# Performance work log

Hardware: AMD Instinct MI355X
Metric: run time of the kernel (lower is better)

The kernel has to match this reference:

```python
import jax, jax.numpy as jnp
import numpy as np

# ---- config matching init_kwargs ----
B, D, U = 8192, 1024, 512
F, E, T = 4, 4, 2
MAX_VAL = 10000000000.0
MIN_VAL = -10000000000.0
DISC_IDX = np.array([[0, 1, 2, 3], [4, 5, 6, 7]])  # discrete fields 0,1: per-expert feature index
CONT_IDX = np.array([8, 9])                         # continuous fields 2,3: single feature index
BOUNDS = np.array([-0.5, 0.0, 0.5])                 # 3 boundaries -> 4 buckets per continuous field
LOWERS = np.concatenate([[MIN_VAL], BOUNDS]).astype(np.float32)
UPPERS = np.concatenate([BOUNDS, [MAX_VAL]]).astype(np.float32)


def setup_inputs() -> dict:
    key = jax.random.key(0)
    ks = jax.random.split(key, 8)
    s_in = 1.0 / np.sqrt(D)
    s_cat = 1.0 / np.sqrt(2 * U)
    x = jax.random.normal(ks[0], (B, D), dtype=jnp.float32)
    Wc = jax.random.normal(ks[1], (D, U), dtype=jnp.float32) * s_in      # common expert kernel
    bc = jnp.zeros((U,), dtype=jnp.float32)
    We = jax.random.normal(ks[2], (F, E, D, U), dtype=jnp.float32) * s_in  # per-field per-expert kernels
    be = jnp.zeros((F, E, U), dtype=jnp.float32)
    Wg = jax.random.normal(ks[3], (T, D, F + 1), dtype=jnp.float32) * s_in  # per-task gate kernels
    bg = jnp.zeros((T, F + 1), dtype=jnp.float32)
    Wa = jax.random.normal(ks[4], (F, 2 * U, 1), dtype=jnp.float32) * s_cat  # attention kernels
    ba = jnp.zeros((F, 1), dtype=jnp.float32)
    Wu = jax.random.normal(ks[5], (F, 2 * U, 1), dtype=jnp.float32) * s_cat  # update kernels
    bu = jnp.zeros((F, 1), dtype=jnp.float32)
    return {"x": x, "Wc": Wc, "bc": bc, "We": We, "be": be,
            "Wg": Wg, "bg": bg, "Wa": Wa, "ba": ba, "Wu": Wu, "bu": bu}


def _field_masks(x):
    # discrete fields: expert j active iff x[:, idx[i][j]] > 0
    m_disc = x[:, DISC_IDX] > 0.0                         # [B, 2, E]
    # continuous fields: bucket x[:, idx] by boundaries (lower < v <= upper)
    v = x[:, CONT_IDX][..., None]                         # [B, 2, 1]
    m_cont = (v > LOWERS) & (v <= UPPERS)                 # [B, 2, E]
    return jnp.concatenate([m_disc, m_cont], axis=1).astype(x.dtype)  # [B, F, E]


def reference(x, Wc, bc, We, be, Wg, bg, Wa, ba, Wu, bu):
    # common expert: [B, U]
    common = jax.nn.relu(x @ Wc + bc)
    # all field experts at once: [B, F, E, U]
    e = jax.nn.relu(jnp.einsum('bd,fedu->bfeu', x, We) + be)
    mask = _field_masks(x)                                # [B, F, E]
    # mask-select active expert(s) per field: [B, F, U]
    field_out = jnp.einsum('bfe,bfeu->bfu', mask, e)
    # concat [common, field] per field: [B, F, 2U]
    cat = jnp.concatenate(
        [jnp.broadcast_to(common[:, None, :], field_out.shape), field_out], axis=-1)
    # sigmoid attention reweights field expert output
    att = jax.nn.sigmoid(jnp.einsum('bfk,fko->bfo', cat, Wa) + ba[None])   # [B, F, 1]
    field_att = att * field_out
    # sigmoid update gate blends field expert with common expert
    upd = jax.nn.sigmoid(jnp.einsum('bfk,fko->bfo', cat, Wu) + bu[None])   # [B, F, 1]
    field_final = upd * field_att + (1.0 - upd) * common[:, None, :]       # [B, F, U]
    # experts = [common] + per-field outputs: [B, F+1, U]
    experts = jnp.concatenate([common[:, None, :], field_final], axis=1)
    # per-task softmax gates over F+1 experts: [B, T, F+1]
    gates = jax.nn.softmax(jnp.einsum('bd,tdg->btg', x, Wg) + bg[None], axis=-1)
    # task outputs: [B, T, U]
    return jnp.einsum('btg,bgu->btu', gates, experts)
```

## Files before the change

### kernel.cpp

```cpp
#include <hip/hip_runtime.h>

typedef unsigned short ushort_t;

#define B_SZ 8192
#define D_SZ 1024
#define U_SZ 512
#define F_SZ 4
#define E_SZ 4
#define T_SZ 2

typedef __attribute__((ext_vector_type(8))) short bf16x8;
typedef __attribute__((ext_vector_type(4))) float f32x4;
typedef __attribute__((ext_vector_type(8))) unsigned short u16x8;

__device__ __forceinline__ unsigned short f2bf(float f) {
  union { float f; unsigned int u; } v; v.f = f;
  unsigned int r = v.u + 0x7FFFu + ((v.u >> 16) & 1u);
  return (unsigned short)(r >> 16);
}
__device__ __forceinline__ float bf2f(unsigned short h) {
  union { unsigned int u; float f; } v; v.u = ((unsigned int)h) << 16;
  return v.f;
}

__device__ __forceinline__ void gload_lds16(const void* g, void* l) {
  __builtin_amdgcn_global_load_lds(
      (const __attribute__((address_space(1))) unsigned int*)g,
      (__attribute__((address_space(3))) unsigned int*)l, 16, 0, 0);
}

__global__ __launch_bounds__(256) void conv_x(const float* __restrict__ x,
                                              ushort_t* __restrict__ xbf,
                                              float* __restrict__ mask) {
  const size_t i = ((size_t)blockIdx.x * 256 + threadIdx.x) * 8;
  const float4 a = *(const float4*)(x + i);
  const float4 c = *(const float4*)(x + i + 4);
  u16x8 o;
  o[0] = f2bf(a.x); o[1] = f2bf(a.y); o[2] = f2bf(a.z); o[3] = f2bf(a.w);
  o[4] = f2bf(c.x); o[5] = f2bf(c.y); o[6] = f2bf(c.z); o[7] = f2bf(c.w);
  *(u16x8*)(xbf + i) = o;

  if ((threadIdx.x & 127) == 0) {
    const int b = blockIdx.x * 2 + (threadIdx.x >> 7);
    const float* xr = x + (size_t)b * D_SZ;
    float m[16];
    m[0] = a.x > 0.f ? 1.f : 0.f; m[1] = a.y > 0.f ? 1.f : 0.f;
    m[2] = a.z > 0.f ? 1.f : 0.f; m[3] = a.w > 0.f ? 1.f : 0.f;
    m[4] = c.x > 0.f ? 1.f : 0.f; m[5] = c.y > 0.f ? 1.f : 0.f;
    m[6] = c.z > 0.f ? 1.f : 0.f; m[7] = c.w > 0.f ? 1.f : 0.f;
    const float LO[4] = {-1e10f, -0.5f, 0.f, 0.5f};
    const float HI[4] = {-0.5f, 0.f, 0.5f, 1e10f};
    const float v0 = xr[8], v1 = xr[9];
#pragma unroll
    for (int j = 0; j < 4; ++j) {
      m[8 + j]  = ((v0 > LO[j]) && (v0 <= HI[j])) ? 1.f : 0.f;
      m[12 + j] = ((v1 > LO[j]) && (v1 <= HI[j])) ? 1.f : 0.f;
    }
#pragma unroll
    for (int k = 0; k < 4; ++k) {
      float4 v4 = {m[k * 4], m[k * 4 + 1], m[k * 4 + 2], m[k * 4 + 3]};
      *(float4*)(mask + (size_t)b * 16 + k * 4) = v4;
    }
  }
}

__global__ __launch_bounds__(256) void conv_w(const float* __restrict__ Wc,
                                              const float* __restrict__ We,
                                              ushort_t* __restrict__ wbf) {
  const int blk = blockIdx.x;
  const int midx = blk >> 7;
  const int tid = blk & 127;
  const int trow = (tid >> 3) * 64;
  const int tcol = (tid & 7) * 64;
  const float* src = (midx == 0) ? Wc : (We + (size_t)(midx - 1) * D_SZ * U_SZ);
  ushort_t* dst = wbf + (size_t)midx * U_SZ * D_SZ;

  __shared__ float tile[64][69];
  const int t = threadIdx.x;
  const int r0 = t >> 2;
  const int cseg = (t & 3) * 16;
#pragma unroll
  for (int j = 0; j < 4; ++j) {
    const float4 v = *(const float4*)(src + (size_t)(trow + r0) * U_SZ + tcol + cseg + j * 4);
    tile[r0][cseg + j * 4 + 0] = v.x;
    tile[r0][cseg + j * 4 + 1] = v.y;
    tile[r0][cseg + j * 4 + 2] = v.z;
    tile[r0][cseg + j * 4 + 3] = v.w;
  }
  __syncthreads();
  const int u = t >> 2;
  const int d0 = (t & 3) * 16;
#pragma unroll
  for (int h = 0; h < 2; ++h) {
    u16x8 ov;
#pragma unroll
    for (int k = 0; k < 8; ++k) ov[k] = f2bf(tile[d0 + h * 8 + k][u]);
    *(u16x8*)(dst + (size_t)(tcol + u) * D_SZ + trow + d0 + h * 8) = ov;
  }
}

__global__ __launch_bounds__(256) void gates_k(const float* __restrict__ x,
                                               const float* __restrict__ Wg,
                                               const float* __restrict__ bg,
                                               float* __restrict__ gates) {
  __shared__ float wgT[10 * 1024];
  const int t = threadIdx.x;
#pragma unroll
  for (int j = 0; j < 40; ++j) {
    const int i = j * 256 + t;
    const int t2 = i / 5120;
    const int rem = i - t2 * 5120;
    const int d = rem / 5;
    const int g = rem - d * 5;
    wgT[(t2 * 5 + g) * 1024 + d] = Wg[i];
  }
  __syncthreads();
  const int lane = t & 63;
  const int w = t >> 6;
#pragma unroll
  for (int rr = 0; rr < 2; ++rr) {
    const int b = blockIdx.x * 8 + w * 2 + rr;
    const float* xr = x + (size_t)b * D_SZ;
    float p[10];
#pragma unroll
    for (int j = 0; j < 10; ++j) p[j] = 0.f;
#pragma unroll
    for (int i = 0; i < 4; ++i) {
      const int d0 = i * 256 + lane * 4;
      const float4 xv = *(const float4*)(xr + d0);
#pragma unroll
      for (int g = 0; g < 10; ++g) {
        const float4 wv = *(const float4*)(wgT + g * 1024 + d0);
        p[g] += xv.x * wv.x + xv.y * wv.y + xv.z * wv.z + xv.w * wv.w;
      }
    }
#pragma unroll
    for (int off = 32; off > 0; off >>= 1)
#pragma unroll
      for (int j = 0; j < 10; ++j) p[j] += __shfl_xor(p[j], off);
    float l[10];
#pragma unroll
    for (int j = 0; j < 10; ++j) l[j] = p[j] + bg[j];
    const float mx0 = fmaxf(fmaxf(fmaxf(l[0], l[1]), fmaxf(l[2], l[3])), l[4]);
    const float mx1 = fmaxf(fmaxf(fmaxf(l[5], l[6]), fmaxf(l[7], l[8])), l[9]);
    float ev[10]; float s0 = 0.f, s1 = 0.f;
#pragma unroll
    for (int g = 0; g < 5; ++g) { ev[g] = expf(l[g] - mx0); s0 += ev[g]; }
#pragma unroll
    for (int g = 5; g < 10; ++g) { ev[g] = expf(l[g] - mx1); s1 += ev[g]; }
    if (lane < 5) gates[(size_t)b * 10 + lane] = ev[lane] / s0;
    else if (lane < 10) gates[(size_t)b * 10 + lane] = ev[lane] / s1;
  }
}

__global__ __launch_bounds__(256, 2) void gemm_fused(
    const ushort_t* __restrict__ xbf, const ushort_t* __restrict__ wbf,
    const float* __restrict__ mask, const float* __restrict__ bc,
    const float* __restrict__ be,
    ushort_t* __restrict__ common, ushort_t* __restrict__ fout) {
  __shared__ ushort_t Ash[128 * 64];
  __shared__ ushort_t Bsh[128 * 64];
  __shared__ float mk[128 * 4];

  const int t = threadIdx.x;
  const int lane = t & 63;
  const int w = t >> 6;
  const int wm = w >> 1;
  const int wn = w & 1;
  const int quad = lane >> 4;
  const int l16 = lane & 15;
  const int m0 = blockIdx.x * 128;
  const int grp = blockIdx.y;
  const bool isCommon = grp >= 16;
  const int f = isCommon ? 0 : (grp >> 2);
  const int uc = isCommon ? (grp - 16) : (grp & 3);
  const int u0 = uc * 128;
  const int nExp = isCommon ? 1 : 4;
  const int midx0 = isCommon ? 0 : (1 + f * 4);

  if (!isCommon && t < 128)
    *(float4*)(&mk[t * 4]) = *(const float4*)(mask + (size_t)(m0 + t) * 16 + f * 4);

  int offs[4];
#pragma unroll
  for (int i = 0; i < 4; ++i) {
    const int c = (w * 4 + i) * 64 + lane;
    const int r = c >> 3;
    const int gc = (c & 7) ^ (r & 7);
    offs[i] = r * D_SZ + gc * 8;
  }
  const ushort_t* xbase = xbf + (size_t)m0 * D_SZ;

  int rowA[4], rowB[4];
#pragma unroll
  for (int i = 0; i < 4; ++i) {
    rowA[i] = wm * 64 + i * 16 + l16;
    rowB[i] = wn * 64 + i * 16 + l16;
  }
  int sw[2];
  sw[0] = ((quad) ^ (l16 & 7)) * 8;
  sw[1] = ((4 + quad) ^ (l16 & 7)) * 8;

  const f32x4 fzero = {0.f, 0.f, 0.f, 0.f};
  f32x4 facc[4][4];
#pragma unroll
  for (int mi = 0; mi < 4; ++mi)
#pragma unroll
    for (int ni = 0; ni < 4; ++ni) facc[mi][ni] = fzero;

  for (int e = 0; e < nExp; ++e) {
    const ushort_t* wbase = wbf + (size_t)(midx0 + e) * (U_SZ * D_SZ) + (size_t)u0 * D_SZ;
    f32x4 acc[4][4];
#pragma unroll
    for (int mi = 0; mi < 4; ++mi)
#pragma unroll
      for (int ni = 0; ni < 4; ++ni) acc[mi][ni] = fzero;

    for (int k0 = 0; k0 < D_SZ; k0 += 64) {
#pragma unroll
      for (int i = 0; i < 4; ++i) {
        gload_lds16(xbase + offs[i] + k0, (char*)Ash + (w * 4 + i) * 1024);
        gload_lds16(wbase + offs[i] + k0, (char*)Bsh + (w * 4 + i) * 1024);
      }
      __syncthreads();
#pragma unroll
      for (int qs = 0; qs < 2; ++qs) {
        bf16x8 av[4], bv[4];
#pragma unroll
        for (int mi = 0; mi < 4; ++mi)
          av[mi] = *(const bf16x8*)(Ash + rowA[mi] * 64 + sw[qs]);
#pragma unroll
        for (int ni = 0; ni < 4; ++ni)
          bv[ni] = *(const bf16x8*)(Bsh + rowB[ni] * 64 + sw[qs]);
#pragma unroll
        for (int mi = 0; mi < 4; ++mi)
#pragma unroll
          for (int ni = 0; ni < 4; ++ni)
            acc[mi][ni] = __builtin_amdgcn_mfma_f32_16x16x32_bf16(av[mi], bv[ni],
                                                                  acc[mi][ni], 0, 0, 0);
      }
      __syncthreads();
    }

    if (isCommon) {
#pragma unroll
      for (int mi = 0; mi < 4; ++mi) {
        const int rowb = m0 + wm * 64 + mi * 16 + quad * 4;
#pragma unroll
        for (int ni = 0; ni < 4; ++ni) {
          const int u = u0 + wn * 64 + ni * 16 + l16;
          const float bcv = bc[u];
#pragma unroll
          for (int r = 0; r < 4; ++r) {
            const float v = fmaxf(acc[mi][ni][r] + bcv, 0.f);
            common[(size_t)(rowb + r) * U_SZ + u] = f2bf(v);
          }
        }
      }
    } else {
#pragma unroll
      for (int ni = 0; ni < 4; ++ni) {
        const int u = u0 + wn * 64 + ni * 16 + l16;
        const float bev = be[(f * 4 + e) * U_SZ + u];
#pragma unroll
        for (int mi = 0; mi < 4; ++mi) {
          const int rowl = wm * 64 + mi * 16 + quad * 4;
#pragma unroll
          for (int r = 0; r < 4; ++r) {
            const float mval = mk[(rowl + r) * 4 + e];
            const float v = fmaxf(acc[mi][ni][r] + bev, 0.f);
            facc[mi][ni][r] += mval * v;
          }
        }
      }
    }
  }

  if (!isCommon) {
#pragma unroll
    for (int mi = 0; mi < 4; ++mi) {
      const int rowl = wm * 64 + mi * 16 + quad * 4;
#pragma unroll
      for (int ni = 0; ni < 4; ++ni) {
        const int u = u0 + wn * 64 + ni * 16 + l16;
#pragma unroll
        for (int r = 0; r < 4; ++r)
          fout[((size_t)(m0 + rowl + r) * F_SZ + f) * U_SZ + u] = f2bf(facc[mi][ni][r]);
      }
    }
  }
}

__global__ __launch_bounds__(256) void stage2_k(
    const ushort_t* __restrict__ common, const ushort_t* __restrict__ fout,
    const float* __restrict__ gates,
    const float* __restrict__ Wa, const float* __restrict__ ba,
    const float* __restrict__ Wu, const float* __restrict__ bu,
    float* __restrict__ out) {
  const int b = blockIdx.x;
  const int t = threadIdx.x;
  const int lane = t & 63;
  const int w = t >> 6;

  const float c0 = bf2f(common[(size_t)b * U_SZ + t]);
  const float c1 = bf2f(common[(size_t)b * U_SZ + 256 + t]);
  float fo0[4], fo1[4];
#pragma unroll
  for (int f = 0; f < 4; ++f) {
    fo0[f] = bf2f(fout[((size_t)b * F_SZ + f) * U_SZ + t]);
    fo1[f] = bf2f(fout[((size_t)b * F_SZ + f) * U_SZ + 256 + t]);
  }
  float pa[4], pu[4];
#pragma unroll
  for (int f = 0; f < 4; ++f) {
    const float* wa = Wa + f * 1024;
    pa[f] = c0 * wa[t] + c1 * wa[256 + t] + fo0[f] * wa[512 + t] + fo1[f] * wa[768 + t];
    const float* wu = Wu + f * 1024;
    pu[f] = c0 * wu[t] + c1 * wu[256 + t] + fo0[f] * wu[512 + t] + fo1[f] * wu[768 + t];
  }
#pragma unroll
  for (int off = 32; off > 0; off >>= 1) {
#pragma unroll
    for (int f = 0; f < 4; ++f) {
      pa[f] += __shfl_xor(pa[f], off);
      pu[f] += __shfl_xor(pu[f], off);
    }
  }
  __shared__ float redA[4][4];
  __shared__ float redU[4][4];
  __shared__ float gsh[10];
  if (lane == 0) {
#pragma unroll
    for (int f = 0; f < 4; ++f) { redA[w][f] = pa[f]; redU[w][f] = pu[f]; }
  }
  if (t < 10) gsh[t] = gates[(size_t)b * 10 + t];
  __syncthreads();
  float att[4], upd[4], ff0[4], ff1[4];
#pragma unroll
  for (int f = 0; f < 4; ++f) {
    const float sa = redA[0][f] + redA[1][f] + redA[2][f] + redA[3][f] + ba[f];
    const float su = redU[0][f] + redU[1][f] + redU[2][f] + redU[3][f] + bu[f];
    att[f] = 1.f / (1.f + expf(-sa));
    upd[f] = 1.f / (1.f + expf(-su));
    ff0[f] = upd[f] * (att[f] * fo0[f]) + (1.f - upd[f]) * c0;
    ff1[f] = upd[f] * (att[f] * fo1[f]) + (1.f - upd[f]) * c1;
  }
#pragma unroll
  for (int t2 = 0; t2 < 2; ++t2) {
    float v0 = gsh[t2 * 5] * c0;
    float v1 = gsh[t2 * 5] * c1;
#pragma unroll
    for (int f = 0; f < 4; ++f) {
      v0 += gsh[t2 * 5 + 1 + f] * ff0[f];
      v1 += gsh[t2 * 5 + 1 + f] * ff1[f];
    }
    out[((size_t)b * T_SZ + t2) * U_SZ + t] = v0;
    out[((size_t)b * T_SZ + t2) * U_SZ + 256 + t] = v1;
  }
}

extern "C" void kernel_launch(void* const* d_in, const int* in_sizes, int n_in,
                              void* d_out, int out_size, void* d_ws, size_t ws_size,
                              hipStream_t stream) {
  (void)in_sizes; (void)n_in; (void)out_size; (void)ws_size;
  const float* x  = (const float*)d_in[0];
  const float* Wc = (const float*)d_in[1];
  const float* bc = (const float*)d_in[2];
  const float* We = (const float*)d_in[3];
  const float* be = (const float*)d_in[4];
  const float* Wg = (const float*)d_in[5];
  const float* bg = (const float*)d_in[6];
  const float* Wa = (const float*)d_in[7];
  const float* ba = (const float*)d_in[8];
  const float* Wu = (const float*)d_in[9];
  const float* bu = (const float*)d_in[10];
  float* out = (float*)d_out;
  char* ws = (char*)d_ws;

  const size_t O_XBF    = 0;
  const size_t O_WBF    = O_XBF + (size_t)B_SZ * D_SZ * 2;
  const size_t O_MASK   = O_WBF + (size_t)17 * U_SZ * D_SZ * 2;
  const size_t O_GATES  = O_MASK + (size_t)B_SZ * 16 * 4;
  const size_t O_COMMON = O_GATES + (size_t)B_SZ * 10 * 4;
  const size_t O_FOUT   = O_COMMON + (size_t)B_SZ * U_SZ * 2;

  ushort_t* xbf    = (ushort_t*)(ws + O_XBF);
  ushort_t* wbf    = (ushort_t*)(ws + O_WBF);
  float*    maskp  = (float*)(ws + O_MASK);
  float*    gatesp = (float*)(ws + O_GATES);
  ushort_t* commonp= (ushort_t*)(ws + O_COMMON);
  ushort_t* foutp  = (ushort_t*)(ws + O_FOUT);

  conv_x<<<dim3(4096), dim3(256), 0, stream>>>(x, xbf, maskp);
  conv_w<<<dim3(17 * 128), dim3(256), 0, stream>>>(Wc, We, wbf);
  gates_k<<<dim3(1024), dim3(256), 0, stream>>>(x, Wg, bg, gatesp);
  gemm_fused<<<dim3(64, 20), dim3(256), 0, stream>>>(xbf, wbf, maskp, bc, be, commonp, foutp);
  stage2_k<<<dim3(8192), dim3(256), 0, stream>>>(commonp, foutp, gatesp, Wa, ba, Wu, bu, out);
}
```

Measured before the change: 328.4 us.

## Group rows by active-expert pattern and compute only active experts per field

```diff
diff --git a/kernel.cpp b/kernel.cpp
--- a/kernel.cpp
+++ b/kernel.cpp
@@ -29,9 +29,15 @@
       (__attribute__((address_space(3))) unsigned int*)l, 16, 0, 0);
 }
 
+__global__ __launch_bounds__(64) void zero_k(int* __restrict__ cnt) {
+  cnt[threadIdx.x] = 0;
+}
+
 __global__ __launch_bounds__(256) void conv_x(const float* __restrict__ x,
                                               ushort_t* __restrict__ xbf,
-                                              float* __restrict__ mask) {
+                                              unsigned int* __restrict__ pat,
+                                              int* __restrict__ rowidx,
+                                              int* __restrict__ cnt) {
   const size_t i = ((size_t)blockIdx.x * 256 + threadIdx.x) * 8;
   const float4 a = *(const float4*)(x + i);
   const float4 c = *(const float4*)(x + i + 4);
@@ -43,24 +49,46 @@
   if ((threadIdx.x & 127) == 0) {
     const int b = blockIdx.x * 2 + (threadIdx.x >> 7);
     const float* xr = x + (size_t)b * D_SZ;
-    float m[16];
-    m[0] = a.x > 0.f ? 1.f : 0.f; m[1] = a.y > 0.f ? 1.f : 0.f;
-    m[2] = a.z > 0.f ? 1.f : 0.f; m[3] = a.w > 0.f ? 1.f : 0.f;
-    m[4] = c.x > 0.f ? 1.f : 0.f; m[5] = c.y > 0.f ? 1.f : 0.f;
-    m[6] = c.z > 0.f ? 1.f : 0.f; m[7] = c.w > 0.f ? 1.f : 0.f;
+    int p0 = 0, p1 = 0, p2 = 0, p3 = 0;
+    p0 |= (a.x > 0.f) << 0; p0 |= (a.y > 0.f) << 1;
+    p0 |= (a.z > 0.f) << 2; p0 |= (a.w > 0.f) << 3;
+    p1 |= (c.x > 0.f) << 0; p1 |= (c.y > 0.f) << 1;
+    p1 |= (c.z > 0.f) << 2; p1 |= (c.w > 0.f) << 3;
     const float LO[4] = {-1e10f, -0.5f, 0.f, 0.5f};
     const float HI[4] = {-0.5f, 0.f, 0.5f, 1e10f};
     const float v0 = xr[8], v1 = xr[9];
 #pragma unroll
     for (int j = 0; j < 4; ++j) {
-      m[8 + j]  = ((v0 > LO[j]) && (v0 <= HI[j])) ? 1.f : 0.f;
-      m[12 + j] = ((v1 > LO[j]) && (v1 <= HI[j])) ? 1.f : 0.f;
-    }
-#pragma unroll
-    for (int k = 0; k < 4; ++k) {
-      float4 v4 = {m[k * 4], m[k * 4 + 1], m[k * 4 + 2], m[k * 4 + 3]};
-      *(float4*)(mask + (size_t)b * 16 + k * 4) = v4;
-    }
+      if ((v0 > LO[j]) && (v0 <= HI[j])) p2 = 1 << j;
+      if ((v1 > LO[j]) && (v1 <= HI[j])) p3 = 1 << j;
+    }
+    pat[b] = (unsigned int)(p0 | (p1 << 4) | (p2 << 8) | (p3 << 12));
+    int pp[4] = {p0, p1, p2, p3};
+#pragma unroll
+    for (int f = 0; f < 4; ++f) {
+      if (pp[f]) {
+        const int pos = atomicAdd(&cnt[f * 16 + pp[f]], 1);
+        rowidx[((size_t)f * 16 + pp[f]) * B_SZ + pos] = b;
+      }
+    }
+  }
+}
+
+__global__ __launch_bounds__(64) void dir_k(const int* __restrict__ cnt,
+                                            int* __restrict__ dir,
+                                            int* __restrict__ ntiles) {
+  const int f = threadIdx.x;
+  if (f < 4) {
+    int idx = 0;
+    for (int pop = 4; pop >= 1; --pop) {
+      for (int p = 1; p < 16; ++p) {
+        if (__popc(p) != pop) continue;
+        const int n = cnt[f * 16 + p];
+        const int nt = (n + 127) >> 7;
+        for (int k = 0; k < nt; ++k) dir[f * 80 + idx++] = p | (k << 8);
+      }
+    }
+    ntiles[f] = idx;
   }
 }
 
@@ -153,14 +181,15 @@
   }
 }
 
-__global__ __launch_bounds__(256, 2) void gemm_fused(
+__global__ __launch_bounds__(256, 2) void gemm2(
     const ushort_t* __restrict__ xbf, const ushort_t* __restrict__ wbf,
-    const float* __restrict__ mask, const float* __restrict__ bc,
-    const float* __restrict__ be,
+    const int* __restrict__ rowidx, const int* __restrict__ cnt,
+    const int* __restrict__ dir, const int* __restrict__ ntiles,
+    const float* __restrict__ bc, const float* __restrict__ be,
     ushort_t* __restrict__ common, ushort_t* __restrict__ fout) {
   __shared__ ushort_t Ash[128 * 64];
   __shared__ ushort_t Bsh[128 * 64];
-  __shared__ float mk[128 * 4];
+  __shared__ int ridx[128];
 
   const int t = threadIdx.x;
   const int lane = t & 63;
@@ -169,27 +198,40 @@
   const int wn = w & 1;
   const int quad = lane >> 4;
   const int l16 = lane & 15;
-  const int m0 = blockIdx.x * 128;
-  const int grp = blockIdx.y;
-  const bool isCommon = grp >= 16;
-  const int f = isCommon ? 0 : (grp >> 2);
-  const int uc = isCommon ? (grp - 16) : (grp & 3);
-  const int u0 = uc * 128;
-  const int nExp = isCommon ? 1 : 4;
-  const int midx0 = isCommon ? 0 : (1 + f * 4);
-
-  if (!isCommon && t < 128)
-    *(float4*)(&mk[t * 4]) = *(const float4*)(mask + (size_t)(m0 + t) * 16 + f * 4);
-
-  int offs[4];
+  const int f = blockIdx.y;
+  const int slot = blockIdx.x;
+  const int u0 = blockIdx.z * 128;
+  const bool isCommon = (f == 4);
+
+  int p = 0, nrows = 128;
+  if (isCommon) {
+    if (slot >= 64) return;
+    if (t < 128) ridx[t] = slot * 128 + t;
+  } else {
+    if (slot >= ntiles[f]) return;
+    const int entry = dir[f * 80 + slot];
+    p = entry & 15;
+    const int tw = entry >> 8;
+    const int n = cnt[f * 16 + p];
+    const int rbase = tw * 128;
+    nrows = min(128, n - rbase);
+    if (t < 128) {
+      const int rr = rbase + ((t < nrows) ? t : 0);
+      ridx[t] = rowidx[((size_t)f * 16 + p) * B_SZ + rr];
+    }
+  }
+  __syncthreads();
+
+  size_t aoff[4]; int boff[4]; int ldsoff[4];
 #pragma unroll
   for (int i = 0; i < 4; ++i) {
     const int c = (w * 4 + i) * 64 + lane;
     const int r = c >> 3;
     const int gc = (c & 7) ^ (r & 7);
-    offs[i] = r * D_SZ + gc * 8;
-  }
-  const ushort_t* xbase = xbf + (size_t)m0 * D_SZ;
+    aoff[i] = (size_t)ridx[r] * D_SZ + gc * 8;
+    boff[i] = r * D_SZ + gc * 8;
+    ldsoff[i] = (w * 4 + i) * 1024;
+  }
 
   int rowA[4], rowB[4];
 #pragma unroll
@@ -201,6 +243,14 @@
   sw[0] = ((quad) ^ (l16 & 7)) * 8;
   sw[1] = ((4 + quad) ^ (l16 & 7)) * 8;
 
+  int elist[4]; int ne = 0;
+  if (isCommon) { elist[0] = 0; ne = 1; }
+  else {
+#pragma unroll
+    for (int e = 0; e < 4; ++e)
+      if (p & (1 << e)) elist[ne++] = e;
+  }
+
   const f32x4 fzero = {0.f, 0.f, 0.f, 0.f};
   f32x4 facc[4][4];
 #pragma unroll
@@ -208,8 +258,9 @@
 #pragma unroll
     for (int ni = 0; ni < 4; ++ni) facc[mi][ni] = fzero;
 
-  for (int e = 0; e < nExp; ++e) {
-    const ushort_t* wbase = wbf + (size_t)(midx0 + e) * (U_SZ * D_SZ) + (size_t)u0 * D_SZ;
+  for (int ei = 0; ei < ne; ++ei) {
+    const int midx = isCommon ? 0 : (1 + f * 4 + elist[ei]);
+    const ushort_t* wbase = wbf + (size_t)midx * (U_SZ * D_SZ) + (size_t)u0 * D_SZ;
     f32x4 acc[4][4];
 #pragma unroll
     for (int mi = 0; mi < 4; ++mi)
@@ -219,8 +270,8 @@
     for (int k0 = 0; k0 < D_SZ; k0 += 64) {
 #pragma unroll
       for (int i = 0; i < 4; ++i) {
-        gload_lds16(xbase + offs[i] + k0, (char*)Ash + (w * 4 + i) * 1024);
-        gload_lds16(wbase + offs[i] + k0, (char*)Bsh + (w * 4 + i) * 1024);
+        gload_lds16(xbf + aoff[i] + k0, (char*)Ash + ldsoff[i]);
+        gload_lds16(wbase + boff[i] + k0, (char*)Bsh + ldsoff[i]);
       }
       __syncthreads();
 #pragma unroll
@@ -245,7 +296,7 @@
     if (isCommon) {
 #pragma unroll
       for (int mi = 0; mi < 4; ++mi) {
-        const int rowb = m0 + wm * 64 + mi * 16 + quad * 4;
+        const int rowb = slot * 128 + wm * 64 + mi * 16 + quad * 4;
 #pragma unroll
         for (int ni = 0; ni < 4; ++ni) {
           const int u = u0 + wn * 64 + ni * 16 + l16;
@@ -258,42 +309,42 @@
         }
       }
     } else {
+      const float* bevp = be + (size_t)(f * 4 + elist[ei]) * U_SZ;
 #pragma unroll
       for (int ni = 0; ni < 4; ++ni) {
         const int u = u0 + wn * 64 + ni * 16 + l16;
-        const float bev = be[(f * 4 + e) * U_SZ + u];
-#pragma unroll
-        for (int mi = 0; mi < 4; ++mi) {
-          const int rowl = wm * 64 + mi * 16 + quad * 4;
-#pragma unroll
-          for (int r = 0; r < 4; ++r) {
-            const float mval = mk[(rowl + r) * 4 + e];
-            const float v = fmaxf(acc[mi][ni][r] + bev, 0.f);
-            facc[mi][ni][r] += mval * v;
+        const float bev = bevp[u];
+#pragma unroll
+        for (int mi = 0; mi < 4; ++mi)
+#pragma unroll
+          for (int r = 0; r < 4; ++r)
+            facc[mi][ni][r] += fmaxf(acc[mi][ni][r] + bev, 0.f);
+      }
+    }
+  }
+
+  if (!isCommon) {
+#pragma unroll
+    for (int mi = 0; mi < 4; ++mi) {
+      const int rowl = wm * 64 + mi * 16 + quad * 4;
+#pragma unroll
+      for (int r = 0; r < 4; ++r) {
+        if (rowl + r < nrows) {
+          const int brow = ridx[rowl + r];
+#pragma unroll
+          for (int ni = 0; ni < 4; ++ni) {
+            const int u = u0 + wn * 64 + ni * 16 + l16;
+            fout[((size_t)brow * F_SZ + f) * U_SZ + u] = f2bf(facc[mi][ni][r]);
           }
         }
       }
     }
   }
-
-  if (!isCommon) {
-#pragma unroll
-    for (int mi = 0; mi < 4; ++mi) {
-      const int rowl = wm * 64 + mi * 16 + quad * 4;
-#pragma unroll
-      for (int ni = 0; ni < 4; ++ni) {
-        const int u = u0 + wn * 64 + ni * 16 + l16;
-#pragma unroll
-        for (int r = 0; r < 4; ++r)
-          fout[((size_t)(m0 + rowl + r) * F_SZ + f) * U_SZ + u] = f2bf(facc[mi][ni][r]);
-      }
-    }
-  }
 }
 
 __global__ __launch_bounds__(256) void stage2_k(
     const ushort_t* __restrict__ common, const ushort_t* __restrict__ fout,
-    const float* __restrict__ gates,
+    const unsigned int* __restrict__ pat, const float* __restrict__ gates,
     const float* __restrict__ Wa, const float* __restrict__ ba,
     const float* __restrict__ Wu, const float* __restrict__ bu,
     float* __restrict__ out) {
@@ -301,14 +352,16 @@
   const int t = threadIdx.x;
   const int lane = t & 63;
   const int w = t >> 6;
+  const unsigned int pv = pat[b];
 
   const float c0 = bf2f(common[(size_t)b * U_SZ + t]);
   const float c1 = bf2f(common[(size_t)b * U_SZ + 256 + t]);
   float fo0[4], fo1[4];
 #pragma unroll
   for (int f = 0; f < 4; ++f) {
-    fo0[f] = bf2f(fout[((size_t)b * F_SZ + f) * U_SZ + t]);
-    fo1[f] = bf2f(fout[((size_t)b * F_SZ + f) * U_SZ + 256 + t]);
+    const bool act = ((pv >> (4 * f)) & 15u) != 0u;
+    fo0[f] = act ? bf2f(fout[((size_t)b * F_SZ + f) * U_SZ + t]) : 0.f;
+    fo1[f] = act ? bf2f(fout[((size_t)b * F_SZ + f) * U_SZ + 256 + t]) : 0.f;
   }
   float pa[4], pu[4];
 #pragma unroll
@@ -335,15 +388,15 @@
   }
   if (t < 10) gsh[t] = gates[(size_t)b * 10 + t];
   __syncthreads();
-  float att[4], upd[4], ff0[4], ff1[4];
+  float ff0[4], ff1[4];
 #pragma unroll
   for (int f = 0; f < 4; ++f) {
     const float sa = redA[0][f] + redA[1][f] + redA[2][f] + redA[3][f] + ba[f];
     const float su = redU[0][f] + redU[1][f] + redU[2][f] + redU[3][f] + bu[f];
-    att[f] = 1.f / (1.f + expf(-sa));
-    upd[f] = 1.f / (1.f + expf(-su));
-    ff0[f] = upd[f] * (att[f] * fo0[f]) + (1.f - upd[f]) * c0;
-    ff1[f] = upd[f] * (att[f] * fo1[f]) + (1.f - upd[f]) * c1;
+    const float att = 1.f / (1.f + expf(-sa));
+    const float upd = 1.f / (1.f + expf(-su));
+    ff0[f] = upd * (att * fo0[f]) + (1.f - upd) * c0;
+    ff1[f] = upd * (att * fo1[f]) + (1.f - upd) * c1;
   }
 #pragma unroll
   for (int t2 = 0; t2 < 2; ++t2) {
@@ -379,21 +432,33 @@
 
   const size_t O_XBF    = 0;
   const size_t O_WBF    = O_XBF + (size_t)B_SZ * D_SZ * 2;
-  const size_t O_MASK   = O_WBF + (size_t)17 * U_SZ * D_SZ * 2;
-  const size_t O_GATES  = O_MASK + (size_t)B_SZ * 16 * 4;
+  const size_t O_PAT    = O_WBF + (size_t)17 * U_SZ * D_SZ * 2;
+  const size_t O_ROWIDX = O_PAT + (size_t)B_SZ * 4;
+  const size_t O_CNT    = O_ROWIDX + (size_t)4 * 16 * B_SZ * 4;
+  const size_t O_DIR    = O_CNT + 256;
+  const size_t O_NT     = O_DIR + 1280;
+  const size_t O_GATES  = O_NT + 16;
   const size_t O_COMMON = O_GATES + (size_t)B_SZ * 10 * 4;
   const size_t O_FOUT   = O_COMMON + (size_t)B_SZ * U_SZ * 2;
 
-  ushort_t* xbf    = (ushort_t*)(ws + O_XBF);
-  ushort_t* wbf    = (ushort_t*)(ws + O_WBF);
-  float*    maskp  = (float*)(ws + O_MASK);
-  float*    gatesp = (float*)(ws + O_GATES);
-  ushort_t* commonp= (ushort_t*)(ws + O_COMMON);
-  ushort_t* foutp  = (ushort_t*)(ws + O_FOUT);
-
-  conv_x<<<dim3(4096), dim3(256), 0, stream>>>(x, xbf, maskp);
+  ushort_t* xbf     = (ushort_t*)(ws + O_XBF);
+  ushort_t* wbf     = (ushort_t*)(ws + O_WBF);
+  unsigned int* patp= (unsigned int*)(ws + O_PAT);
+  int*      rowidxp = (int*)(ws + O_ROWIDX);
+  int*      cntp    = (int*)(ws + O_CNT);
+  int*      dirp    = (int*)(ws + O_DIR);
+  int*      ntp     = (int*)(ws + O_NT);
+  float*    gatesp  = (float*)(ws + O_GATES);
+  ushort_t* commonp = (ushort_t*)(ws + O_COMMON);
+  ushort_t* foutp   = (ushort_t*)(ws + O_FOUT);
+
+  zero_k<<<dim3(1), dim3(64), 0, stream>>>(cntp);
+  conv_x<<<dim3(4096), dim3(256), 0, stream>>>(x, xbf, patp, rowidxp, cntp);
+  dir_k<<<dim3(1), dim3(64), 0, stream>>>(cntp, dirp, ntp);
   conv_w<<<dim3(17 * 128), dim3(256), 0, stream>>>(Wc, We, wbf);
   gates_k<<<dim3(1024), dim3(256), 0, stream>>>(x, Wg, bg, gatesp);
-  gemm_fused<<<dim3(64, 20), dim3(256), 0, stream>>>(xbf, wbf, maskp, bc, be, commonp, foutp);
-  stage2_k<<<dim3(8192), dim3(256), 0, stream>>>(commonp, foutp, gatesp, Wa, ba, Wu, bu, out);
-}
+  gemm2<<<dim3(80, 5, 4), dim3(256), 0, stream>>>(xbf, wbf, rowidxp, cntp, dirp, ntp,
+                                                  bc, be, commonp, foutp);
+  stage2_k<<<dim3(8192), dim3(256), 0, stream>>>(commonp, foutp, patp, gatesp,
+                                                 Wa, ba, Wu, bu, out);
+}
```

After: 512.9 us. 56.2% more time.
